# Performance work log

Measured on AMD Instinct MI355X. Metric: run time of the kernel, lower is better.

The kernel has to match this reference:

```python
import jax, jax.numpy as jnp
import numpy as np

BN_EPS = 1e-3  # Keras BatchNormalization default epsilon


def _conv_block(x, k):
    """Per-task conv (stride 2, pad 1) -> ReLU -> BatchNorm (center/scale=False, training).

    x: [B, E, H, W, Cin]  (B tasks, E examples per task)
    k: [B, kh, kw, Cin, Cout]  per-task kernel
    """
    def conv_one(xe, kt):  # xe: [E,H,W,Cin], kt: [kh,kw,Cin,Cout]
        return jax.lax.conv_general_dilated(
            xe, kt, window_strides=(2, 2), padding=[(1, 1), (1, 1)],
            dimension_numbers=('NHWC', 'HWIO', 'NHWC'))
    y = jax.nn.relu(jax.vmap(conv_one)(x, k))  # [B,E,H',W',Cout]
    # BatchNorm in training mode: moments over all axes except channels
    m = jnp.mean(y, axis=(0, 1, 2, 3))
    v = jnp.var(y, axis=(0, 1, 2, 3))
    return (y - m) * jax.lax.rsqrt(v + BN_EPS)


def setup_inputs() -> dict:
    key = jax.random.key(0)
    ks = jax.random.split(key, 6)
    B, E, H, C, O = 64, 64, 28, 64, 20
    return {
        'x': jax.random.normal(ks[0], (B, E, H, H, 1), dtype=jnp.float32),
        'k1': jax.random.normal(ks[1], (B, 3, 3, 1, C), dtype=jnp.float32) * 0.1,
        'k2': jax.random.normal(ks[2], (B, 3, 3, C, C), dtype=jnp.float32) * 0.05,
        'k3': jax.random.normal(ks[3], (B, 3, 3, C, C), dtype=jnp.float32) * 0.05,
        'k4': jax.random.normal(ks[4], (B, 3, 3, C, C), dtype=jnp.float32) * 0.05,
        'w_ro': jax.random.normal(ks[5], (B, C, O), dtype=jnp.float32) * 0.1,
    }


def reference(x, k1, k2, k3, k4, w_ro):
    h = _conv_block(x, k1)   # [B,E,14,14,C]
    h = _conv_block(h, k2)   # [B,E,7,7,C]
    h = _conv_block(h, k3)   # [B,E,4,4,C]
    h = _conv_block(h, k4)   # [B,E,2,2,C]
    # MaxPooling2D with pool size == full spatial extent -> global spatial max
    feat = jnp.max(h, axis=(2, 3))  # [B,E,C]
    # per-task readout matmul: [B,E,H] x [B,H,O] -> [B,E,O]
    return jnp.einsum('beh,bho->beo', feat, w_ro)
```

## Files before the change

kernel.cpp:

```cpp
#include <hip/hip_runtime.h>

#define BN_EPS 1e-3f

typedef __attribute__((ext_vector_type(8))) short bf16x8;
typedef __attribute__((ext_vector_type(16))) float floatx16;
typedef unsigned short u16;

__device__ __forceinline__ u16 f2bf(float f) {
  unsigned u = __float_as_uint(f);
  u += 0x7fffu + ((u >> 16) & 1u);
  return (u16)(u >> 16);
}
__device__ __forceinline__ float bf2f(u16 h) {
  return __uint_as_float(((unsigned)h) << 16);
}

__device__ __forceinline__ int swzh(int r) { return ((r >> 1) + (r >> 3)) & 7; }

static constexpr int NSHARD = 64;

__global__ __launch_bounds__(256, 4) void conv1_k(
    const float* __restrict__ x, const float* __restrict__ k1,
    u16* __restrict__ y1, float* __restrict__ statsSh)
{
  __shared__ __align__(16) u16 smem1[15360];
  __shared__ __align__(16) float xp[30 * 36];
  __shared__ float redsum[64], redss[64];

  u16* Ah = smem1;
  u16* Al = smem1 + 6144;
  u16* Wh = smem1 + 12288;
  u16* Wl = smem1 + 13824;

  const int be = blockIdx.x, b = be >> 6, tid = threadIdx.x;

  {
    const uint4 z = uint4{0, 0, 0, 0};
    for (int i = tid; i < 1920; i += 256) ((uint4*)smem1)[i] = z;
    for (int i = tid; i < 270; i += 256) ((uint4*)xp)[i] = z;
    if (tid < 64) { redsum[tid] = 0.f; redss[tid] = 0.f; }
  }
  __syncthreads();

  for (int i = tid; i < 784; i += 256) {
    const int r = i / 28, c = i - 28 * r;
    xp[(r + 1) * 36 + (c + 1)] = x[(size_t)be * 784 + i];
  }
  for (int idx = tid; idx < 576; idx += 256) {
    const int t = idx >> 6, c = idx & 63;
    const float v = k1[(size_t)b * 576 + idx];
    const u16 hi = f2bf(v);
    const u16 lo = f2bf(v - bf2f(hi));
    Wh[c * 24 + t] = hi;
    Wl[c * 24 + t] = lo;
  }
  __syncthreads();

  if (tid < 196) {
    const int oy = tid / 14, ox = tid - 14 * oy;
    const float* base = &xp[(2 * oy) * 36 + 2 * ox];
#pragma unroll
    for (int ky = 0; ky < 3; ++ky)
#pragma unroll
      for (int kx = 0; kx < 3; ++kx) {
        const float v = base[ky * 36 + kx];
        const u16 hi = f2bf(v);
        const u16 lo = f2bf(v - bf2f(hi));
        Ah[tid * 24 + ky * 3 + kx] = hi;
        Al[tid * 24 + ky * 3 + kx] = lo;
      }
  }
  __syncthreads();

  const int wave = tid >> 6, lane = tid & 63;
  const int l31 = lane & 31, kq = (lane >> 5) * 8;

  bf16x8 ah[2], al[2], bh[2], bl[2];
#pragma unroll
  for (int mt = 0; mt < 2; ++mt) {
    const int row = (wave * 2 + mt) * 32 + l31;
    ah[mt] = *(const bf16x8*)&Ah[row * 24 + kq];
    al[mt] = *(const bf16x8*)&Al[row * 24 + kq];
  }
#pragma unroll
  for (int nt = 0; nt < 2; ++nt) {
    const int colB = nt * 32 + l31;
    bh[nt] = *(const bf16x8*)&Wh[colB * 24 + kq];
    bl[nt] = *(const bf16x8*)&Wl[colB * 24 + kq];
  }

  floatx16 acc[2][2];
#pragma unroll
  for (int mt = 0; mt < 2; ++mt)
#pragma unroll
    for (int nt = 0; nt < 2; ++nt) {
#pragma unroll
      for (int r = 0; r < 16; ++r) acc[mt][nt][r] = 0.f;
      acc[mt][nt] = __builtin_amdgcn_mfma_f32_32x32x16_bf16(
          al[mt], bh[nt], acc[mt][nt], 0, 0, 0);
      acc[mt][nt] = __builtin_amdgcn_mfma_f32_32x32x16_bf16(
          ah[mt], bl[nt], acc[mt][nt], 0, 0, 0);
      acc[mt][nt] = __builtin_amdgcn_mfma_f32_32x32x16_bf16(
          ah[mt], bh[nt], acc[mt][nt], 0, 0, 0);
    }

  __syncthreads();
  u16* yS = smem1;

#pragma unroll
  for (int nt = 0; nt < 2; ++nt) {
    const int col = nt * 32 + l31;
    float ls = 0.f, lss = 0.f;
#pragma unroll
    for (int mt = 0; mt < 2; ++mt) {
      const int rb = (wave * 2 + mt) * 32 + 4 * (lane >> 5);
#pragma unroll
      for (int r = 0; r < 16; ++r) {
        const int rw = rb + (r & 3) + 8 * (r >> 2);
        if (rw < 196) {
          const float v = fmaxf(acc[mt][nt][r], 0.f);
          yS[rw * 64 + col] = f2bf(v);
          ls += v;
          lss = fmaf(v, v, lss);
        }
      }
    }
    atomicAdd(&redsum[col], ls);
    atomicAdd(&redss[col], lss);
  }
  __syncthreads();

  {
    uint4* dst = (uint4*)(y1 + (size_t)be * 12544);
    const uint4* s4 = (const uint4*)yS;
    for (int i = tid; i < 1568; i += 256) dst[i] = s4[i];
  }
  if (tid < 64) {
    const int sh = be & (NSHARD - 1);
    atomicAdd(&statsSh[sh * 128 + tid], redsum[tid]);
    atomicAdd(&statsSh[sh * 128 + 64 + tid], redss[tid]);
  }
}

__global__ __launch_bounds__(256) void foldw_k(
    const float* __restrict__ W, const float* __restrict__ statsSh, float invN,
    u16* __restrict__ Wf, float* __restrict__ biasCls)
{
  __shared__ float T[64 * 68];
  __shared__ float P[256];
  __shared__ float s1[64], t1[64];
  __shared__ float tbS[64];

  const int b = blockIdx.x / 3, sg = blockIdx.x % 3;
  const int tid = threadIdx.x;

  {
    const int g = tid >> 7, cidx = tid & 127;
    float acc = 0.f;
    for (int k = 0; k < NSHARD / 2; ++k)
      acc += statsSh[(g * (NSHARD / 2) + k) * 128 + cidx];
    P[tid] = acc;
  }
  __syncthreads();
  if (tid < 64) {
    const float m = (P[tid] + P[tid + 128]) * invN;
    const float var = fmaf(-m, m, (P[64 + tid] + P[192 + tid]) * invN);
    const float s = rsqrtf(var + BN_EPS);
    s1[tid] = s;
    t1[tid] = -m * s;
  }
  __syncthreads();

  const int cin = tid >> 2, q0 = (tid & 3) * 16;
  const int cout = tid >> 2, ci0 = (tid & 3) * 16;
  for (int s = sg * 3; s < sg * 3 + 3; ++s) {
    if (tid < 64) tbS[tid] = 0.f;
    const float* ss = W + ((size_t)b * 9 + s) * 4096;
#pragma unroll
    for (int q = 0; q < 16; q += 4) {
      const float4 v = *(const float4*)(ss + cin * 64 + q0 + q);
      T[(q0 + q + 0) * 68 + cin] = v.x;
      T[(q0 + q + 1) * 68 + cin] = v.y;
      T[(q0 + q + 2) * 68 + cin] = v.z;
      T[(q0 + q + 3) * 68 + cin] = v.w;
    }
    __syncthreads();
    alignas(16) u16 tmp[16];
    float tb = 0.f;
#pragma unroll
    for (int j = 0; j < 16; ++j) {
      const float wv = T[cout * 68 + ci0 + j];
      tmp[j] = f2bf(wv * s1[ci0 + j]);
      tb = fmaf(t1[ci0 + j], wv, tb);
    }
    u16* dst = Wf + ((size_t)b * 9 + s) * 4096 + cout * 64 + ci0;
    *(uint4*)dst       = *(uint4*)&tmp[0];
    *(uint4*)(dst + 8) = *(uint4*)&tmp[8];
    atomicAdd(&tbS[cout], tb);
    __syncthreads();
    if (tid < 64) {
      const int ky = s / 3, kx = s % 3;
      const float tv = tbS[tid];
#pragma unroll
      for (int cls = 0; cls < 9; ++cls) {
        const int ry = cls / 3, rx = cls % 3;
        const bool valid = !((ry == 1 && ky == 0) || (ry == 2 && ky == 2) ||
                             (rx == 1 && kx == 0) || (rx == 2 && kx == 2));
        if (valid) atomicAdd(&biasCls[(size_t)b * 576 + cls * 64 + tid], tv);
      }
    }
    __syncthreads();
  }
}

template <int Hin, int Hout, int G>
__device__ __forceinline__ void conv_core(
    const u16* __restrict__ yin, const u16* __restrict__ Wf,
    const float* __restrict__ biasCls, u16* __restrict__ yout,
    float* __restrict__ statsSh, int blk)
{
  constexpr int PPI  = Hout * Hout;
  constexpr int ROWS = G * PPI;
  constexpr int BPT  = 64 / G;
  constexpr int MR   = G * Hin * Hin;
  constexpr int ZR   = MR;

  __shared__ __align__(16) u16 mapS[(MR + 1) * 64];
  __shared__ float biasS[576];
  __shared__ float redsum[64], redss[64];

  const int b = blk / BPT, e0 = (blk % BPT) * G;
  const int tid = threadIdx.x, lane = tid & 63, wave = tid >> 6;

  for (int i = tid; i < 576; i += 256) biasS[i] = biasCls[(size_t)b * 576 + i];
  if (tid < 64) { redsum[tid] = 0.f; redss[tid] = 0.f; }
  if (tid < 8) *(uint4*)&mapS[(ZR << 6) + (tid << 3)] = uint4{0, 0, 0, 0};

  {
    const u16* src = yin + (size_t)(b * 64 + e0) * (Hin * Hin) * 64;
    for (int ch = tid; ch < MR * 8; ch += 256) {
      const int r = ch >> 3, c8 = ch & 7;
      const int sc = c8 ^ swzh(r);
      *(uint4*)&mapS[(r << 6) + (sc << 3)] = *(const uint4*)(src + ch * 8);
    }
  }

  const int m0 = (wave & 1) * 32, n0 = (wave >> 1) * 32;
  const int l31 = lane & 31, kh = lane >> 5;
  const int lrow = m0 + l31;
  const bool rv = lrow < ROWS;
  const int img = rv ? lrow / PPI : 0;
  const int pp  = rv ? lrow % PPI : 0;
  const int oy = pp / Hout, ox = pp % Hout;

  const u16* wbase = Wf + (size_t)b * 9 * 4096 + (n0 + l31) * 64 + kh * 8;

  bf16x8 bq[2][4];
#pragma unroll
  for (int ps = 0; ps < 2; ++ps)
#pragma unroll
    for (int kk = 0; kk < 4; ++kk)
      bq[ps][kk] = *(const bf16x8*)(wbase + ps * 4096 + kk * 16);

  floatx16 acc;
#pragma unroll
  for (int r = 0; r < 16; ++r) acc[r] = 0.f;

  __syncthreads();

#pragma unroll
  for (int s = 0; s < 9; ++s) {
    const int ky = s / 3, kx = s % 3;
    int pix = ZR;
    if (rv) {
      const int iy = 2 * oy - 1 + ky, ix = 2 * ox - 1 + kx;
      if ((unsigned)iy < (unsigned)Hin && (unsigned)ix < (unsigned)Hin)
        pix = img * (Hin * Hin) + iy * Hin + ix;
    }
    const int hh = swzh(pix);
    const int abase = pix << 6;
    bf16x8 a[4];
#pragma unroll
    for (int kk = 0; kk < 4; ++kk)
      a[kk] = *(const bf16x8*)&mapS[abase + (((kh + 2 * kk) ^ hh) << 3)];
#pragma unroll
    for (int kk = 0; kk < 4; ++kk)
      acc = __builtin_amdgcn_mfma_f32_32x32x16_bf16(a[kk], bq[s & 1][kk],
                                                    acc, 0, 0, 0);
    if (s < 7) {
#pragma unroll
      for (int kk = 0; kk < 4; ++kk)
        bq[s & 1][kk] = *(const bf16x8*)(wbase + (s + 2) * 4096 + kk * 16);
    }
  }

  const int col = n0 + l31;
  const int rb = m0 + 4 * (lane >> 5);
  float ls = 0.f, lss = 0.f;
#pragma unroll
  for (int r = 0; r < 16; ++r) {
    const int rw = rb + (r & 3) + 8 * (r >> 2);
    if (rw < ROWS) {
      const int re = rw / PPI, pr = rw % PPI;
      const int ooy = pr / Hout, oox = pr % Hout;
      const int ry = (ooy == 0) ? 1 : ((2 * ooy + 1 >= Hin) ? 2 : 0);
      const int rx = (oox == 0) ? 1 : ((2 * oox + 1 >= Hin) ? 2 : 0);
      const float v = fmaxf(acc[r] + biasS[(ry * 3 + rx) * 64 + col], 0.f);
      yout[((size_t)(b * 64 + e0 + re) * PPI + pr) * 64 + col] = f2bf(v);
      ls += v;
      lss = fmaf(v, v, lss);
    }
  }
  atomicAdd(&redsum[col], ls);
  atomicAdd(&redss[col], lss);
  __syncthreads();
  if (tid < 64) {
    const int sh = blk & (NSHARD - 1);
    atomicAdd(&statsSh[sh * 128 + tid], redsum[tid]);
    atomicAdd(&statsSh[sh * 128 + 64 + tid], redss[tid]);
  }
}

__global__ __launch_bounds__(256, 4) void cg2_k(
    const u16* __restrict__ yin, const u16* __restrict__ Wf,
    const float* __restrict__ biasCls, u16* __restrict__ yout,
    float* __restrict__ statsSh) {
  conv_core<14, 7, 1>(yin, Wf, biasCls, yout, statsSh, blockIdx.x);
}
__global__ __launch_bounds__(256, 4) void cg3_k(
    const u16* __restrict__ yin, const u16* __restrict__ Wf,
    const float* __restrict__ biasCls, u16* __restrict__ yout,
    float* __restrict__ statsSh) {
  conv_core<7, 4, 4>(yin, Wf, biasCls, yout, statsSh, blockIdx.x);
}
__global__ __launch_bounds__(256, 4) void cg4_k(
    const u16* __restrict__ yin, const u16* __restrict__ Wf,
    const float* __restrict__ biasCls, u16* __restrict__ yout,
    float* __restrict__ statsSh) {
  conv_core<4, 2, 16>(yin, Wf, biasCls, yout, statsSh, blockIdx.x);
}

__global__ __launch_bounds__(256) void readout_k(
    const u16* __restrict__ y4, const float* __restrict__ w_ro,
    const float* __restrict__ statsSh, float invN, float* __restrict__ outp)
{
  __shared__ float wl[64 * 20];
  __shared__ float feat[64 * 64];
  __shared__ float P[256];
  __shared__ float sArr[64], tArr[64];

  const int b = blockIdx.x, tid = threadIdx.x;

  {
    const int g = tid >> 7, cidx = tid & 127;
    float acc = 0.f;
    for (int k = 0; k < NSHARD / 2; ++k)
      acc += statsSh[(g * (NSHARD / 2) + k) * 128 + cidx];
    P[tid] = acc;
  }
  for (int i = tid; i < 1280; i += 256) wl[i] = w_ro[(size_t)b * 1280 + i];
  __syncthreads();
  if (tid < 64) {
    const float m = (P[tid] + P[tid + 128]) * invN;
    const float var = fmaf(-m, m, (P[64 + tid] + P[192 + tid]) * invN);
    const float s = rsqrtf(var + BN_EPS);
    sArr[tid] = s;
    tArr[tid] = -m * s;
  }
  __syncthreads();

  {
    const int e = tid & 63;
    for (int c = tid >> 6; c < 64; c += 4) {
      const u16* p4 = y4 + ((size_t)(b * 64 + e) * 4) * 64 + c;
      const float v = fmaxf(fmaxf(bf2f(p4[0]), bf2f(p4[64])),
                            fmaxf(bf2f(p4[128]), bf2f(p4[192])));
      feat[c * 64 + e] = fmaf(v, sArr[c], tArr[c]);
    }
  }
  __syncthreads();

  const int e = tid >> 2, og = (tid & 3) * 5;
  float acc[5] = {0.f, 0.f, 0.f, 0.f, 0.f};
  for (int c = 0; c < 64; ++c) {
    const float f = feat[c * 64 + e];
#pragma unroll
    for (int j = 0; j < 5; ++j) acc[j] = fmaf(f, wl[c * 20 + og + j], acc[j]);
  }
#pragma unroll
  for (int j = 0; j < 5; ++j)
    outp[((size_t)b * 64 + e) * 20 + og + j] = acc[j];
}

extern "C" void kernel_launch(void* const* d_in, const int* in_sizes, int n_in,
                              void* d_out, int out_size, void* d_ws, size_t ws_size,
                              hipStream_t stream) {
  (void)in_sizes; (void)n_in; (void)out_size; (void)ws_size;
  const float* x   = (const float*)d_in[0];
  const float* k1  = (const float*)d_in[1];
  const float* k2  = (const float*)d_in[2];
  const float* k3  = (const float*)d_in[3];
  const float* k4  = (const float*)d_in[4];
  const float* wro = (const float*)d_in[5];
  float* out = (float*)d_out;
  char* ws = (char*)d_ws;

  float* stats = (float*)ws;
  float* bias2 = (float*)(ws + 131072);
  float* bias3 = bias2 + 36864;
  float* bias4 = bias3 + 36864;
  u16* k2f = (u16*)(ws + 131072 + 442368);
  u16* k3f = k2f + (size_t)2359296;
  u16* k4f = k3f + (size_t)2359296;
  u16* y2 = k4f + (size_t)2359296;
  u16* y1 = y2 + (size_t)12845056;
  u16* y3 = y1;
  u16* y4 = y3 + (size_t)4194304;

  float* st1 = stats;
  float* st2 = stats + 8192;
  float* st3 = stats + 16384;
  float* st4 = stats + 24576;

  hipMemsetAsync(stats, 0, 131072 + 442368, stream);

  conv1_k<<<4096, 256, 0, stream>>>(x, k1, y1, st1);
  foldw_k<<<192, 256, 0, stream>>>(k2, st1, 1.f / 802816.f, k2f, bias2);
  cg2_k<<<4096, 256, 0, stream>>>(y1, k2f, bias2, y2, st2);
  foldw_k<<<192, 256, 0, stream>>>(k3, st2, 1.f / 200704.f, k3f, bias3);
  cg3_k<<<1024, 256, 0, stream>>>(y2, k3f, bias3, y3, st3);
  foldw_k<<<192, 256, 0, stream>>>(k4, st3, 1.f / 65536.f, k4f, bias4);
  cg4_k<<<256, 256, 0, stream>>>(y3, k4f, bias4, y4, st4);
  readout_k<<<64, 256, 0, stream>>>(y4, wro, st4, 1.f / 16384.f, out);
}
```

Measured before the change: 286.1 us.

## Stage conv weights through LDS and use channel-group-major activation layout

Replaces the XOR-swizzled row-major activation tile with a channel-group-major layout (8-channel chunk index outermost), removing the swizzle arithmetic. Weights for each tap are now loaded cooperatively once per block into a shared LDS buffer instead of each wave loading its own fragments from global memory, with a one-step register prefetch. This reduces redundant global weight traffic but adds two block-wide barriers per filter tap, which may serialize the MFMA loop.

Result: faster. 254.0 us (-11.2%).

```diff
diff --git a/kernel.cpp b/kernel.cpp
--- a/kernel.cpp
+++ b/kernel.cpp
@@ -14,8 +14,6 @@
 __device__ __forceinline__ float bf2f(u16 h) {
   return __uint_as_float(((unsigned)h) << 16);
 }
-
-__device__ __forceinline__ int swzh(int r) { return ((r >> 1) + (r >> 3)) & 7; }
 
 static constexpr int NSHARD = 64;
 
@@ -224,8 +222,10 @@
   constexpr int BPT  = 64 / G;
   constexpr int MR   = G * Hin * Hin;
   constexpr int ZR   = MR;
-
-  __shared__ __align__(16) u16 mapS[(MR + 1) * 64];
+  constexpr int MS   = MR + 1;
+
+  __shared__ __align__(16) u16 map2[8 * MS * 8];
+  __shared__ __align__(16) u16 B2[8 * 64 * 8];
   __shared__ float biasS[576];
   __shared__ float redsum[64], redss[64];
 
@@ -234,15 +234,23 @@
 
   for (int i = tid; i < 576; i += 256) biasS[i] = biasCls[(size_t)b * 576 + i];
   if (tid < 64) { redsum[tid] = 0.f; redss[tid] = 0.f; }
-  if (tid < 8) *(uint4*)&mapS[(ZR << 6) + (tid << 3)] = uint4{0, 0, 0, 0};
+  if (tid < 8) *(uint4*)&map2[(tid * MS + ZR) * 8] = uint4{0, 0, 0, 0};
 
   {
     const u16* src = yin + (size_t)(b * 64 + e0) * (Hin * Hin) * 64;
     for (int ch = tid; ch < MR * 8; ch += 256) {
       const int r = ch >> 3, c8 = ch & 7;
-      const int sc = c8 ^ swzh(r);
-      *(uint4*)&mapS[(r << 6) + (sc << 3)] = *(const uint4*)(src + ch * 8);
-    }
+      *(uint4*)&map2[(c8 * MS + r) * 8] = *(const uint4*)(src + ch * 8);
+    }
+  }
+
+  const int bco = tid >> 2, bq0 = (tid & 3) * 16, c8a = bq0 >> 3;
+  const u16* wb = Wf + (size_t)b * 9 * 4096 + bco * 64 + bq0;
+  {
+    uint4 b0 = *(const uint4*)wb;
+    uint4 b1 = *(const uint4*)(wb + 8);
+    *(uint4*)&B2[((c8a + 0) * 64 + bco) * 8] = b0;
+    *(uint4*)&B2[((c8a + 1) * 64 + bco) * 8] = b1;
   }
 
   const int m0 = (wave & 1) * 32, n0 = (wave >> 1) * 32;
@@ -252,15 +260,7 @@
   const int img = rv ? lrow / PPI : 0;
   const int pp  = rv ? lrow % PPI : 0;
   const int oy = pp / Hout, ox = pp % Hout;
-
-  const u16* wbase = Wf + (size_t)b * 9 * 4096 + (n0 + l31) * 64 + kh * 8;
-
-  bf16x8 bq[2][4];
-#pragma unroll
-  for (int ps = 0; ps < 2; ++ps)
-#pragma unroll
-    for (int kk = 0; kk < 4; ++kk)
-      bq[ps][kk] = *(const bf16x8*)(wbase + ps * 4096 + kk * 16);
+  const int bcol = n0 + l31;
 
   floatx16 acc;
 #pragma unroll
@@ -270,6 +270,12 @@
 
 #pragma unroll
   for (int s = 0; s < 9; ++s) {
+    uint4 nb0, nb1;
+    if (s < 8) {
+      const u16* wsl = wb + (s + 1) * 4096;
+      nb0 = *(const uint4*)wsl;
+      nb1 = *(const uint4*)(wsl + 8);
+    }
     const int ky = s / 3, kx = s % 3;
     int pix = ZR;
     if (rv) {
@@ -277,24 +283,25 @@
       if ((unsigned)iy < (unsigned)Hin && (unsigned)ix < (unsigned)Hin)
         pix = img * (Hin * Hin) + iy * Hin + ix;
     }
-    const int hh = swzh(pix);
-    const int abase = pix << 6;
-    bf16x8 a[4];
+    bf16x8 a[4], bv[4];
+#pragma unroll
+    for (int kk = 0; kk < 4; ++kk) {
+      const int c8 = (kk << 1) | kh;
+      a[kk]  = *(const bf16x8*)&map2[(c8 * MS + pix) * 8];
+      bv[kk] = *(const bf16x8*)&B2[(c8 * 64 + bcol) * 8];
+    }
 #pragma unroll
     for (int kk = 0; kk < 4; ++kk)
-      a[kk] = *(const bf16x8*)&mapS[abase + (((kh + 2 * kk) ^ hh) << 3)];
-#pragma unroll
-    for (int kk = 0; kk < 4; ++kk)
-      acc = __builtin_amdgcn_mfma_f32_32x32x16_bf16(a[kk], bq[s & 1][kk],
-                                                    acc, 0, 0, 0);
-    if (s < 7) {
-#pragma unroll
-      for (int kk = 0; kk < 4; ++kk)
-        bq[s & 1][kk] = *(const bf16x8*)(wbase + (s + 2) * 4096 + kk * 16);
-    }
-  }
-
-  const int col = n0 + l31;
+      acc = __builtin_amdgcn_mfma_f32_32x32x16_bf16(a[kk], bv[kk], acc, 0, 0, 0);
+    if (s < 8) {
+      __syncthreads();
+      *(uint4*)&B2[((c8a + 0) * 64 + bco) * 8] = nb0;
+      *(uint4*)&B2[((c8a + 1) * 64 + bco) * 8] = nb1;
+      __syncthreads();
+    }
+  }
+
+  const int col = bcol;
   const int rb = m0 + 4 * (lane >> 5);
   float ls = 0.f, lss = 0.f;
 #pragma unroll
```
